# Performance work log

Hardware: AMD Instinct MI355X
Metric: run time of the kernel (lower is better)

Reference implementation:

```python
import jax, jax.numpy as jnp
import numpy as np

B, S, D, H = 4, 1024, 1024, 16
HD = D // H  # head_dim = 64


def setup_inputs() -> dict:
    key = jax.random.key(0)
    k1, k2, k3, k4 = jax.random.split(key, 4)
    scale = 1.0 / np.sqrt(D)
    return {
        "x": jax.random.normal(k1, (B, S, D), dtype=jnp.float32),
        "w_qkv": jax.random.normal(k2, (3 * D, D), dtype=jnp.float32) * scale,
        "w_out": jax.random.normal(k3, (D, D), dtype=jnp.float32) * scale,
        "b_out": jax.random.normal(k4, (D,), dtype=jnp.float32) * scale,
    }


def reference(x, w_qkv, w_out, b_out):
    b, s, d_model = x.shape
    # qkv linear (no bias): (b, s, 3*D); torch Linear computes x @ W.T
    qkv = x @ w_qkv.T
    # Rearrange 'b s (qkv h hd) -> qkv b h s hd'
    qkv = qkv.reshape(b, s, 3, H, HD).transpose(2, 0, 3, 1, 4)
    q, k, v = qkv[0], qkv[1], qkv[2]
    scale = HD ** -0.5
    att = jax.nn.softmax(jnp.einsum('bhxd,bhyd->bhxy', q, k) * scale, axis=-1)
    out = jnp.einsum('bhxy,bhyd->bhxd', att, v)  # (b, h, s, hd)
    out = out.transpose(0, 2, 1, 3).reshape(b, s, d_model)  # 'b h s hd -> b s (h hd)'
    return out @ w_out.T + b_out
```

## Files before the change

### kernel.cpp

```cpp
#include <hip/hip_runtime.h>
#include <hip/hip_bf16.h>
#include <stdint.h>

typedef unsigned short u16;
typedef __bf16 bf16x8 __attribute__((ext_vector_type(8)));
typedef u16 u16x8 __attribute__((ext_vector_type(8)));
typedef u16 u16x4 __attribute__((ext_vector_type(4)));
typedef float f32x4 __attribute__((ext_vector_type(4)));

#define MFMA_16x16x32(a, b, c) __builtin_amdgcn_mfma_f32_16x16x32_bf16((a), (b), (c), 0, 0, 0)

#if __has_builtin(__builtin_amdgcn_exp2f)
#define EXP2F(x) __builtin_amdgcn_exp2f(x)
#else
#define EXP2F(x) exp2f(x)
#endif

#define QSCALE_F 0.18033688011112042f

__device__ __forceinline__ u16 f2b(float f) {
  __bf16 h = (__bf16)f;
  return __builtin_bit_cast(u16, h);
}

__device__ __forceinline__ void store_c(u16* C, size_t idx, float v) { C[idx] = f2b(v); }
__device__ __forceinline__ void store_c(float* C, size_t idx, float v) { C[idx] = v; }

__device__ __forceinline__ void gload16(const void* g, void* l) {
  __builtin_amdgcn_global_load_lds(
      (const __attribute__((address_space(1))) unsigned int*)(uintptr_t)(g),
      (__attribute__((address_space(3))) unsigned int*)(uintptr_t)(l),
      16, 0, 0);
}

template <int N> __device__ __forceinline__ void wait_vmcnt();
#define DEF_WAITVM(N)                                          \
  template <> __device__ __forceinline__ void wait_vmcnt<N>() { \
    asm volatile("s_waitcnt vmcnt(" #N ")" ::: "memory");       \
    __builtin_amdgcn_sched_barrier(0);                          \
  }
DEF_WAITVM(0) DEF_WAITVM(3) DEF_WAITVM(4) DEF_WAITVM(5) DEF_WAITVM(8)

__device__ __forceinline__ void wait_lgkm0() {
  asm volatile("s_waitcnt lgkmcnt(0)" ::: "memory");
  __builtin_amdgcn_sched_barrier(0);
}

template <typename T, int ROWS>
__device__ __forceinline__ void stage_tile(const T* __restrict__ G, int ldg, int tr, int k0,
                                           T* Ls, int wave, int lane) {
  constexpr int EPL = 16 / sizeof(T);
  constexpr int PCE = 64 * EPL;
  constexpr int CALLS = (ROWS * 32) / (4 * PCE);
#pragma unroll
  for (int ci = 0; ci < CALLS; ci++) {
    const int base = (wave * CALLS + ci) * PCE;
    const int idx0 = base + lane * EPL;
    const int r = idx0 >> 5;
    const int c = idx0 & 31;
    int csw;
    if constexpr (sizeof(T) == 2)
      csw = ((c >> 3) ^ (r & 3)) << 3;
    else
      csw = ((c >> 2) ^ (r & 7)) << 2;
    gload16(G + (size_t)(tr + r) * ldg + k0 + csw, Ls + base);
  }
}
template <typename T, int ROWS>
struct stage_calls {
  static constexpr int value = (ROWS * 32) / (4 * 64 * (16 / (int)sizeof(T)));
};

__device__ __forceinline__ bf16x8 load_frag_sw(const u16* Ls, int row, int g8) {
  const int c = ((g8 >> 3) ^ (row & 3)) << 3;
  return *(const bf16x8*)(Ls + row * 32 + c);
}
__device__ __forceinline__ bf16x8 load_frag_sw(const float* Ls, int row, int g8) {
  const int g2 = g8 >> 2;
  const int c0 = (g2 ^ (row & 7)) << 2;
  const int c1 = ((g2 + 1) ^ (row & 7)) << 2;
  f32x4 lo = *(const f32x4*)(Ls + row * 32 + c0);
  f32x4 hi = *(const f32x4*)(Ls + row * 32 + c1);
  bf16x8 r;
#pragma unroll
  for (int e = 0; e < 4; e++) {
    r[e] = (__bf16)lo[e];
    r[e + 4] = (__bf16)hi[e];
  }
  return r;
}

template <typename TA, typename TB, typename TC, bool BIAS, bool QSC, int TM>
__global__ __launch_bounds__(256, 2) void gemm_bt(const TA* __restrict__ A,
                                                  const TB* __restrict__ B,
                                                  const float* __restrict__ bias,
                                                  TC* __restrict__ C,
                                                  int M, int N, int K) {
  constexpr int MI = TM >> 5;
  constexpr int NL = stage_calls<TA, TM>::value + stage_calls<TB, 128>::value;
  __shared__ TA As[2][TM * 32];
  __shared__ TB Bs[2][128 * 32];
  const int tid = threadIdx.x;
  const int lane = tid & 63;
  const int wave = tid >> 6;
  const int l15 = lane & 15;
  const int g = lane >> 4;
  const int g8 = g * 8;
  const int cpx = (int)gridDim.x >> 3;
  const int xsl = (int)blockIdx.x & 7;
  const int jj = (int)blockIdx.x >> 3;
  const int tiles_n = N >> 7;
  int tmi, tni;
  const int gm = cpx / tiles_n;
  if (gm * tiles_n == cpx) {
    tmi = xsl * gm + (jj % gm);
    tni = jj / gm;
  } else {
    const int bid = xsl * cpx + jj;
    tmi = bid / tiles_n;
    tni = bid % tiles_n;
  }
  const int tm = tmi * TM;
  const int tn = tni << 7;
  const int wm = (wave >> 1) * (TM >> 1);
  const int wn = (wave & 1) << 6;

  f32x4 acc[MI][4] = {};

  const int nt = K >> 5;
  stage_tile<TA, TM>(A, K, tm, 0, As[0], wave, lane);
  stage_tile<TB, 128>(B, K, tn, 0, Bs[0], wave, lane);

  for (int t = 0; t < nt; t++) {
    const int cur = t & 1;
    if (t + 1 < nt) {
      stage_tile<TA, TM>(A, K, tm, (t + 1) << 5, As[cur ^ 1], wave, lane);
      stage_tile<TB, 128>(B, K, tn, (t + 1) << 5, Bs[cur ^ 1], wave, lane);
      wait_vmcnt<NL>();
    } else {
      wait_vmcnt<0>();
    }
    __builtin_amdgcn_s_barrier();
    __builtin_amdgcn_sched_barrier(0);
    bf16x8 af[MI], bfr[4];
#pragma unroll
    for (int i = 0; i < MI; i++) af[i] = load_frag_sw(As[cur], wm + i * 16 + l15, g8);
#pragma unroll
    for (int i = 0; i < 4; i++) bfr[i] = load_frag_sw(Bs[cur], wn + i * 16 + l15, g8);
    wait_lgkm0();
    __builtin_amdgcn_s_barrier();
#pragma unroll
    for (int mi = 0; mi < MI; mi++)
#pragma unroll
      for (int nj = 0; nj < 4; nj++)
        acc[mi][nj] = MFMA_16x16x32(af[mi], bfr[nj], acc[mi][nj]);
  }

  float bv[4], cs[4];
#pragma unroll
  for (int nj = 0; nj < 4; nj++) {
    const int col = tn + wn + nj * 16 + l15;
    bv[nj] = BIAS ? bias[col] : 0.0f;
    cs[nj] = (QSC && col < 1024) ? QSCALE_F : 1.0f;
  }

#pragma unroll
  for (int mi = 0; mi < MI; mi++) {
#pragma unroll
    for (int nj = 0; nj < 4; nj++) {
      const int row = tm + wm + mi * 16 + g * 4;
      const int col = tn + wn + nj * 16 + l15;
#pragma unroll
      for (int r = 0; r < 4; r++)
        store_c(C, (size_t)(row + r) * N + col, (acc[mi][nj][r] + bv[nj]) * cs[nj]);
    }
  }
}

__global__ __launch_bounds__(256) void cvt3(const float* __restrict__ x,
                                            const float* __restrict__ wq,
                                            const float* __restrict__ wo,
                                            u16* __restrict__ xb,
                                            u16* __restrict__ wqb,
                                            u16* __restrict__ wob) {
  const int i = blockIdx.x * 256 + threadIdx.x;
  const float* src;
  u16* dst;
  int k;
  if (i < 524288) {
    src = x;
    dst = xb;
    k = i;
  } else if (i < 524288 + 393216) {
    src = wq;
    dst = wqb;
    k = i - 524288;
  } else {
    src = wo;
    dst = wob;
    k = i - (524288 + 393216);
  }
  const f32x4* p = (const f32x4*)src + (size_t)k * 2;
  f32x4 a = p[0], bq = p[1];
  u16x8 r;
#pragma unroll
  for (int e = 0; e < 4; e++) {
    r[e] = f2b(a[e]);
    r[e + 4] = f2b(bq[e]);
  }
  *((u16x8*)dst + k) = r;
}

__global__ __launch_bounds__(256) void cvt_bf16(const float* __restrict__ in,
                                                u16* __restrict__ out, int n8) {
  const int i = blockIdx.x * 256 + threadIdx.x;
  if (i >= n8) return;
  const f32x4* p = (const f32x4*)in + (size_t)i * 2;
  f32x4 a = p[0], b = p[1];
  u16x8 r;
#pragma unroll
  for (int e = 0; e < 4; e++) {
    r[e] = f2b(a[e]);
    r[e + 4] = f2b(b[e]);
  }
  *((u16x8*)out + i) = r;
}

__device__ __forceinline__ int swz64(int row) { return ((row >> 3) ^ row) & 7; }

__global__ __launch_bounds__(512) void attn(const u16* __restrict__ qkv,
                                            u16* __restrict__ attout) {
  __shared__ u16 Ks[2][64 * 64];
  __shared__ u16 Vs[2][64 * 64];
  __shared__ u16 Pl[8][32 * 64];
  const int tid = threadIdx.x;
  const int lane = tid & 63;
  const int w = tid >> 6;
  const int l15 = lane & 15;
  const int g = lane >> 4;
  const int g8 = g * 8;

  const int bid = blockIdx.x;
  const int xs = bid & 7;
  const int j = bid >> 3;
  const int bh = xs * 8 + (j >> 2);
  const int qt = j & 3;
  const int b = bh >> 4;
  const int h = bh & 15;
  const size_t rowbase = (size_t)b * 1024;
  const int qcol = h * 64;

  const int qr0 = qt * 256 + w * 32;
  bf16x8 qf[2][2];
#pragma unroll
  for (int mi = 0; mi < 2; mi++)
#pragma unroll
    for (int ks = 0; ks < 2; ks++)
      qf[mi][ks] =
          *(const bf16x8*)&qkv[(rowbase + qr0 + mi * 16 + l15) * 3072 + qcol + ks * 32 + g8];

  f32x4 o[2][4] = {};
  float l_r[2][4] = {};

  const int vh3 = tid & 7;
  const int vhc = vh3 << 3;
  const int vkey = tid >> 3;
  bf16x8 vreg;

  auto loadV = [&](int kt) {
    vreg = *(const bf16x8*)&qkv[(rowbase + kt * 64 + vkey) * 3072 + 2048 + qcol + vhc];
  };
  auto writeV = [&](int buf) {
    const int pos = ((vkey & 15) << 2) | (vkey >> 4);
    const u16* vu = (const u16*)&vreg;
#pragma unroll
    for (int e = 0; e < 8; e++) {
      const int sl = (vh3 ^ e) & 7;
      Vs[buf][(vhc + e) * 64 + (pos ^ (sl << 3))] = vu[e];
    }
  };
  auto stageK = [&](int buf, int kt) {
    const int row = w * 8 + (lane >> 3);
    const int cc = (lane & 7) ^ swz64(row);
    gload16(&qkv[(rowbase + kt * 64 + row) * 3072 + 1024 + qcol + cc * 8],
            &Ks[buf][w * 512]);
  };

  stageK(0, 0);
  loadV(0);
  writeV(0);
  __syncthreads();

  for (int kt = 0; kt < 16; kt++) {
    const int cur = kt & 1;
    if (kt < 15) {
      stageK(cur ^ 1, kt + 1);
      loadV(kt + 1);
    }

    f32x4 s[2][4] = {};
    __builtin_amdgcn_s_setprio(1);
#pragma unroll
    for (int nj = 0; nj < 4; nj++) {
      const int key = nj * 16 + l15;
      const int sk = swz64(key) << 3;
#pragma unroll
      for (int ks = 0; ks < 2; ks++) {
        const bf16x8 kfr = *(const bf16x8*)&Ks[cur][key * 64 + ((ks * 32 + g8) ^ sk)];
#pragma unroll
        for (int mi = 0; mi < 2; mi++)
          s[mi][nj] = MFMA_16x16x32(qf[mi][ks], kfr, s[mi][nj]);
      }
    }
    __builtin_amdgcn_s_setprio(0);

#pragma unroll
    for (int mi = 0; mi < 2; mi++)
#pragma unroll
      for (int r = 0; r < 4; r++) {
        const float p0 = EXP2F(s[mi][0][r]);
        const float p1 = EXP2F(s[mi][1][r]);
        const float p2 = EXP2F(s[mi][2][r]);
        const float p3 = EXP2F(s[mi][3][r]);
        l_r[mi][r] += (p0 + p1) + (p2 + p3);
        const int row = mi * 16 + g * 4 + r;
        const int sq = swz64(row) << 3;
        u16x4 pk;
        pk[0] = f2b(p0);
        pk[1] = f2b(p1);
        pk[2] = f2b(p2);
        pk[3] = f2b(p3);
        *(u16x4*)&Pl[w][row * 64 + ((l15 << 2) ^ sq)] = pk;
      }

    bf16x8 pf[2][2];
#pragma unroll
    for (int mi = 0; mi < 2; mi++) {
      const int pr = mi * 16 + l15;
      const int sp = swz64(pr) << 3;
#pragma unroll
      for (int ks = 0; ks < 2; ks++)
        pf[mi][ks] = *(const bf16x8*)&Pl[w][pr * 64 + ((ks * 32 + g8) ^ sp)];
    }
    __builtin_amdgcn_s_setprio(1);
#pragma unroll
    for (int nj = 0; nj < 4; nj++) {
      const int hd = nj * 16 + l15;
      const int sv = swz64(hd) << 3;
#pragma unroll
      for (int ks = 0; ks < 2; ks++) {
        const bf16x8 vf = *(const bf16x8*)&Vs[cur][hd * 64 + ((ks * 32 + g8) ^ sv)];
#pragma unroll
        for (int mi = 0; mi < 2; mi++)
          o[mi][nj] = MFMA_16x16x32(pf[mi][ks], vf, o[mi][nj]);
      }
    }
    __builtin_amdgcn_s_setprio(0);

    if (kt < 15) writeV(cur ^ 1);
    __syncthreads();
  }

#pragma unroll
  for (int mi = 0; mi < 2; mi++)
#pragma unroll
    for (int r = 0; r < 4; r++) {
      float v = l_r[mi][r];
#pragma unroll
      for (int d = 1; d < 16; d <<= 1) v += __shfl_xor(v, d, 64);
      l_r[mi][r] = v;
    }

#pragma unroll
  for (int mi = 0; mi < 2; mi++) {
    float inv[4];
#pragma unroll
    for (int r = 0; r < 4; r++) inv[r] = 1.0f / l_r[mi][r];
#pragma unroll
    for (int nj = 0; nj < 4; nj++)
#pragma unroll
      for (int r = 0; r < 4; r++)
        attout[(rowbase + qr0 + mi * 16 + g * 4 + r) * 1024 + qcol + nj * 16 + l15] =
            f2b(o[mi][nj][r] * inv[r]);
  }
}

extern "C" void kernel_launch(void* const* d_in, const int* in_sizes, int n_in,
                              void* d_out, int out_size, void* d_ws, size_t ws_size,
                              hipStream_t stream) {
  const float* x = (const float*)d_in[0];
  const float* w_qkv = (const float*)d_in[1];
  const float* w_out = (const float*)d_in[2];
  const float* b_out = (const float*)d_in[3];
  float* out = (float*)d_out;

  u16* qkv = (u16*)d_ws;
  u16* attout = qkv + 12582912;
  const size_t needA = 39845888ull;
  const size_t needB = needA + 2097152ull;

  u16* xb = attout;
  u16* wqb = attout + 4194304;

  if (ws_size >= needB) {
    u16* wob = wqb + 3145728;
    cvt3<<<dim3(4096), dim3(256), 0, stream>>>(x, w_qkv, w_out, xb, wqb, wob);
    gemm_bt<u16, u16, u16, false, true, 128><<<dim3(32 * 24), dim3(256), 0, stream>>>(
        xb, wqb, nullptr, qkv, 4096, 3072, 1024);
    attn<<<dim3(256), dim3(512), 0, stream>>>(qkv, attout);
    gemm_bt<u16, u16, float, true, false, 64><<<dim3(64 * 8), dim3(256), 0, stream>>>(
        attout, wob, b_out, out, 4096, 1024, 1024);
  } else if (ws_size >= needA) {
    u16* wob = wqb;
    cvt3<<<dim3(3584), dim3(256), 0, stream>>>(x, w_qkv, w_qkv, xb, wqb, wob);
    gemm_bt<u16, u16, u16, false, true, 128><<<dim3(32 * 24), dim3(256), 0, stream>>>(
        xb, wqb, nullptr, qkv, 4096, 3072, 1024);
    cvt_bf16<<<dim3(512), dim3(256), 0, stream>>>(w_out, wob, 131072);
    attn<<<dim3(256), dim3(512), 0, stream>>>(qkv, attout);
    gemm_bt<u16, u16, float, true, false, 64><<<dim3(64 * 8), dim3(256), 0, stream>>>(
        attout, wob, b_out, out, 4096, 1024, 1024);
  } else {
    gemm_bt<float, float, u16, false, true, 128><<<dim3(32 * 24), dim3(256), 0, stream>>>(
        x, w_qkv, nullptr, qkv, 4096, 3072, 1024);
    attn<<<dim3(256), dim3(512), 0, stream>>>(qkv, attout);
    gemm_bt<u16, float, float, true, false, 64><<<dim3(64 * 8), dim3(256), 0, stream>>>(
        attout, w_out, b_out, out, 4096, 1024, 1024);
  }
}
```

Measured before the change: 90.09 us.

## Process two KV tiles per barrier with quad-buffered K/V shared memory

The attention loop now stages two 64-key tiles of K and V per iteration into four LDS buffers and computes both before a single barrier. This halves the number of __syncthreads calls and gives the global loads more work to overlap with. In exchange, K/V shared memory grows from 32KB to 64KB per block and register use rises for the second V staging register, which can lower occupancy.

```diff
diff --git a/kernel.cpp b/kernel.cpp
--- a/kernel.cpp
+++ b/kernel.cpp
@@ -230,8 +230,8 @@
 
 __global__ __launch_bounds__(512) void attn(const u16* __restrict__ qkv,
                                             u16* __restrict__ attout) {
-  __shared__ u16 Ks[2][64 * 64];
-  __shared__ u16 Vs[2][64 * 64];
+  __shared__ u16 Ks[4][64 * 64];
+  __shared__ u16 Vs[4][64 * 64];
   __shared__ u16 Pl[8][32 * 64];
   const int tid = threadIdx.x;
   const int lane = tid & 63;
@@ -265,14 +265,14 @@
   const int vh3 = tid & 7;
   const int vhc = vh3 << 3;
   const int vkey = tid >> 3;
-  bf16x8 vreg;
-
-  auto loadV = [&](int kt) {
-    vreg = *(const bf16x8*)&qkv[(rowbase + kt * 64 + vkey) * 3072 + 2048 + qcol + vhc];
+  bf16x8 vreg[2];
+
+  auto loadV = [&](int kt, int vr) {
+    vreg[vr] = *(const bf16x8*)&qkv[(rowbase + kt * 64 + vkey) * 3072 + 2048 + qcol + vhc];
   };
-  auto writeV = [&](int buf) {
+  auto writeV = [&](int buf, int vr) {
     const int pos = ((vkey & 15) << 2) | (vkey >> 4);
-    const u16* vu = (const u16*)&vreg;
+    const u16* vu = (const u16*)&vreg[vr];
 #pragma unroll
     for (int e = 0; e < 8; e++) {
       const int sl = (vh3 ^ e) & 7;
@@ -286,18 +286,7 @@
             &Ks[buf][w * 512]);
   };
 
-  stageK(0, 0);
-  loadV(0);
-  writeV(0);
-  __syncthreads();
-
-  for (int kt = 0; kt < 16; kt++) {
-    const int cur = kt & 1;
-    if (kt < 15) {
-      stageK(cur ^ 1, kt + 1);
-      loadV(kt + 1);
-    }
-
+  auto compute = [&](int buf) {
     f32x4 s[2][4] = {};
     __builtin_amdgcn_s_setprio(1);
 #pragma unroll
@@ -306,14 +295,13 @@
       const int sk = swz64(key) << 3;
 #pragma unroll
       for (int ks = 0; ks < 2; ks++) {
-        const bf16x8 kfr = *(const bf16x8*)&Ks[cur][key * 64 + ((ks * 32 + g8) ^ sk)];
+        const bf16x8 kfr = *(const bf16x8*)&Ks[buf][key * 64 + ((ks * 32 + g8) ^ sk)];
 #pragma unroll
         for (int mi = 0; mi < 2; mi++)
           s[mi][nj] = MFMA_16x16x32(qf[mi][ks], kfr, s[mi][nj]);
       }
     }
     __builtin_amdgcn_s_setprio(0);
-
 #pragma unroll
     for (int mi = 0; mi < 2; mi++)
 #pragma unroll
@@ -332,7 +320,6 @@
         pk[3] = f2b(p3);
         *(u16x4*)&Pl[w][row * 64 + ((l15 << 2) ^ sq)] = pk;
       }
-
     bf16x8 pf[2][2];
 #pragma unroll
     for (int mi = 0; mi < 2; mi++) {
@@ -349,15 +336,37 @@
       const int sv = swz64(hd) << 3;
 #pragma unroll
       for (int ks = 0; ks < 2; ks++) {
-        const bf16x8 vf = *(const bf16x8*)&Vs[cur][hd * 64 + ((ks * 32 + g8) ^ sv)];
+        const bf16x8 vf = *(const bf16x8*)&Vs[buf][hd * 64 + ((ks * 32 + g8) ^ sv)];
 #pragma unroll
         for (int mi = 0; mi < 2; mi++)
           o[mi][nj] = MFMA_16x16x32(pf[mi][ks], vf, o[mi][nj]);
       }
     }
     __builtin_amdgcn_s_setprio(0);
-
-    if (kt < 15) writeV(cur ^ 1);
+  };
+
+  stageK(0, 0);
+  stageK(1, 1);
+  loadV(0, 0);
+  loadV(1, 1);
+  writeV(0, 0);
+  writeV(1, 1);
+  __syncthreads();
+
+  for (int kt2 = 0; kt2 < 8; kt2++) {
+    const int t0 = kt2 * 2;
+    if (kt2 < 7) {
+      stageK((t0 + 2) & 3, t0 + 2);
+      stageK((t0 + 3) & 3, t0 + 3);
+      loadV(t0 + 2, 0);
+      loadV(t0 + 3, 1);
+    }
+    compute(t0 & 3);
+    compute((t0 + 1) & 3);
+    if (kt2 < 7) {
+      writeV((t0 + 2) & 3, 0);
+      writeV((t0 + 3) & 3, 1);
+    }
     __syncthreads();
   }
 
```

Measured after the change: 88.39 us. Within noise of the previous version (-1.9%).
